# Optimization experiments

Measured on AMD Instinct MI355X. Metric: run time of the kernel, lower is better.

The kernel has to match this reference:

```python
import jax, jax.numpy as jnp
import numpy as np

B, S, H, D = 2, 2048, 16, 64
BLK_Q, BLK_K = 16, 256  # layout row-block = 16 query rows, col-block = 256 key cols


def setup_inputs() -> dict:
    key = jax.random.key(0)
    qkv = jax.random.normal(key, (B, S, 3, H, D), dtype=jnp.float32)
    nq, nk = S // BLK_Q, S // BLK_K  # 128, 8
    layout = np.zeros((nq, nk), dtype=np.int32)
    rows = np.arange(nq)
    layout[rows, (rows * BLK_Q) // BLK_K] = 1  # local diagonal block
    layout[:, 0] = 1                           # global first key block
    return {"qkv": qkv, "layout": jnp.asarray(layout)}


def reference(qkv, layout):
    # qkv: [B, S, 3, H, D], layout: [S//16, S//256] {0,1}
    b, s, _, h, d = qkv.shape
    scale = 1.0 / np.sqrt(d)  # softmax_temp defaults to 1/sqrt(d_keys)
    q = qkv[:, :, 0]  # [B,S,H,D]
    k = qkv[:, :, 1]
    v = qkv[:, :, 2]
    # Expand block layout to a dense [S, S] boolean mask
    mask = jnp.repeat(jnp.repeat(layout.astype(bool), BLK_Q, axis=0), BLK_K, axis=1)[:s, :s]
    scores = jnp.einsum('bshd,bthd->bhst', q, k) * scale  # [B,H,S,S]
    neg_inf = jnp.asarray(-jnp.inf, scores.dtype)
    scores = jnp.where(mask[None, None], scores, neg_inf)
    attn = jax.nn.softmax(scores, axis=-1)  # dropout_p = 0.0 in eval
    out = jnp.einsum('bhst,bthd->bshd', attn, v)  # [B,S,H,D]
    return out
```

## Files before the change

kernel.cpp:

```cpp
#include <hip/hip_runtime.h>

typedef float f32x4 __attribute__((ext_vector_type(4)));
typedef float f32x16 __attribute__((ext_vector_type(16)));
typedef _Float16 f16x8 __attribute__((ext_vector_type(8)));
typedef __fp16 fp16x2 __attribute__((ext_vector_type(2)));
typedef int i32x2 __attribute__((ext_vector_type(2)));

static __device__ __forceinline__ unsigned pk2(float a, float b) {
    fp16x2 r = __builtin_amdgcn_cvt_pkrtz(a, b);
    return __builtin_bit_cast(unsigned, r);
}
static __device__ __forceinline__ f16x8 pk8(float4 a, float4 b) {
    uint4 u; u.x = pk2(a.x, a.y); u.y = pk2(a.z, a.w);
    u.z = pk2(b.x, b.y); u.w = pk2(b.z, b.w);
    return __builtin_bit_cast(f16x8, u);
}

#define MFMA32(A, B, C) __builtin_amdgcn_mfma_f32_32x32x16_f16((A), (B), (C), 0, 0, 0)

__global__ __launch_bounds__(256, 2) void fba_fwd(const float* __restrict__ qkv,
                                                  const int* __restrict__ layout,
                                                  float* __restrict__ out) {
    __shared__ unsigned short Klds[2][128 * 64];
    __shared__ unsigned short Vtlds[2][64 * 128];

    const int bid = blockIdx.x;
    const int vid = (bid & 7) * 64 + (bid >> 3);
    const int b = vid >> 8;
    const int hh = (vid >> 4) & 15;
    const int j = (vid >> 1) & 7;
    const int qh = vid & 1;

    const int tid = threadIdx.x;
    const int w = tid >> 6;
    const int lane = tid & 63;
    const int l31 = lane & 31;
    const int h = lane >> 5;

    const size_t bbase = (size_t)b * 2048 * 3072;
    const int qbase = 256 * j + 128 * qh + 32 * w;

    unsigned kbl = 0; int nact = 0;
    for (int kb = 0; kb < 8; ++kb) {
        int a = 0;
        #pragma unroll
        for (int r = 0; r < 8; ++r) a |= layout[(16 * j + 8 * qh + r) * 8 + kb];
        if (a) { kbl |= (unsigned)kb << (4 * nact); ++nact; }
    }
    kbl = __builtin_amdgcn_readfirstlane(kbl);
    const int ntile = 2 * nact;

    const float SC = 0.18033688f;
    f16x8 qf[4];
    {
        const float* qp = qkv + bbase + (size_t)(qbase + l31) * 3072 + hh * 64;
        #pragma unroll
        for (int ds = 0; ds < 4; ++ds) {
            const float* p0 = qp + ds * 16 + 8 * h;
            float4 x = *(const float4*)p0;
            float4 y = *(const float4*)(p0 + 4);
            float4 xs = {x.x * SC, x.y * SC, x.z * SC, x.w * SC};
            float4 ys = {y.x * SC, y.y * SC, y.z * SC, y.w * SC};
            qf[ds] = pk8(xs, ys);
        }
    }

    f32x16 acc[2];
    acc[0] = (f32x16)(0.f);
    acc[1] = (f32x16)(0.f);
    float lsum = 0.f;

    const int skey = tid >> 4;
    const int sdc  = tid & 15;

    float4 kr0, kr1, kr2, kr3;
    float4 va0, vb0, va1, vb1;

#define STAGE_LOAD(ks_) {            \
    const float* kp_ = qkv + bbase + (size_t)((ks_) + skey) * 3072 + 1024 + hh * 64 + sdc * 4; \
    kr0 = *(const float4*)kp_;                                                      \
    kr1 = *(const float4*)(kp_ + 16 * 3072);                                        \
    kr2 = *(const float4*)(kp_ + 32 * 3072);                                        \
    kr3 = *(const float4*)(kp_ + 48 * 3072);                                        \
    const float* vp_ = qkv + bbase + (size_t)((ks_) + 2 * skey) * 3072 + 2048 + hh * 64 + sdc * 4; \
    va0 = *(const float4*)vp_;               vb0 = *(const float4*)(vp_ +      3072); \
    va1 = *(const float4*)(vp_ + 32 * 3072); vb1 = *(const float4*)(vp_ + 33 * 3072); \
}

#define WK1(m, krm, KB, koff) { int row_ = (koff) + skey + 16 * (m);                \
    *(uint2*)((char*)(KB) + ((row_ * 128 + sdc * 8) ^ ((skey & 7) << 4))) =         \
        make_uint2(pk2(krm.x, krm.y), pk2(krm.z, krm.w)); }
#define WV1(p, vam, vbm, VB, koff) {                                                \
    const float* A_ = &vam.x; const float* B_ = &vbm.x;                             \
    _Pragma("unroll")                                                               \
    for (int e2 = 0; e2 < 4; ++e2) {                                                \
        int d_ = 4 * sdc + e2;                                                      \
        int off_ = (d_ * 256 + ((koff) + 2 * skey + 32 * (p)) * 2) ^ (((d_ ^ (d_ >> 3)) & 7) << 4); \
        *(unsigned*)((char*)(VB) + off_) = pk2(A_[e2], B_[e2]);                     \
    }                                                                               \
}
#define STAGE_WRITE(nb, koff) {                                                     \
    unsigned short* KB = &Klds[nb][0];                                              \
    WK1(0, kr0, KB, koff) WK1(1, kr1, KB, koff) WK1(2, kr2, KB, koff) WK1(3, kr3, KB, koff) \
    unsigned short* VB = &Vtlds[nb][0];                                             \
    WV1(0, va0, vb0, VB, koff) WV1(1, va1, vb1, VB, koff)                           \
}

#define CHUNK(KB, VB, kt) {                                                         \
    const int key = (kt) * 32 + l31;                                                \
    const int kswz = (l31 & 7) << 4;                                                \
    f16x8 kf[4];                                                                    \
    _Pragma("unroll")                                                               \
    for (int ds = 0; ds < 4; ++ds)                                                  \
        kf[ds] = *(const f16x8*)((const char*)(KB) + ((key * 128 + ds * 32 + h * 16) ^ kswz)); \
    f16x8 vf[2][2];                                                                 \
    _Pragma("unroll")                                                               \
    for (int dt = 0; dt < 2; ++dt) {                                                \
        const int d = dt * 32 + l31;                                                \
        const int vswz = ((d ^ (d >> 3)) & 7) << 4;                                 \
        _Pragma("unroll")                                                           \
        for (int ksi = 0; ksi < 2; ++ksi)                                           \
            vf[dt][ksi] = *(const f16x8*)((const char*)(VB) + ((d * 256 + (kt) * 64 + ksi * 32 + h * 16) ^ vswz)); \
    }                                                                               \
    __builtin_amdgcn_s_setprio(1);                                                  \
    f32x16 st = (f32x16)(0.f);                                                      \
    st = MFMA32(kf[0], qf[0], st);                                                  \
    st = MFMA32(kf[1], qf[1], st);                                                  \
    st = MFMA32(kf[2], qf[2], st);                                                  \
    st = MFMA32(kf[3], qf[3], st);                                                  \
    __builtin_amdgcn_s_setprio(0);                                                  \
    unsigned ulo[4], uhi[4];                                                        \
    float psum = 0.f;                                                               \
    _Pragma("unroll")                                                               \
    for (int jq = 0; jq < 4; ++jq) {                                                \
        float e0 = exp2f(st[4 * jq + 0]), e1 = exp2f(st[4 * jq + 1]);               \
        float e2 = exp2f(st[4 * jq + 2]), e3 = exp2f(st[4 * jq + 3]);               \
        psum += (e0 + e1) + (e2 + e3);                                              \
        ulo[jq] = pk2(e0, e1); uhi[jq] = pk2(e2, e3);                               \
    }                                                                               \
    lsum += psum;                                                                   \
    __builtin_amdgcn_s_setprio(1);                                                  \
    _Pragma("unroll")                                                               \
    for (int ksi = 0; ksi < 2; ++ksi) {                                             \
        i32x2 r0 = __builtin_amdgcn_permlane32_swap((int)ulo[2 * ksi], (int)ulo[2 * ksi + 1], false, false); \
        i32x2 r1 = __builtin_amdgcn_permlane32_swap((int)uhi[2 * ksi], (int)uhi[2 * ksi + 1], false, false); \
        uint4 uw;                                                                   \
        uw.x = (unsigned)r0[0]; uw.y = (unsigned)r1[0];                             \
        uw.z = (unsigned)r0[1]; uw.w = (unsigned)r1[1];                             \
        f16x8 pf = __builtin_bit_cast(f16x8, uw);                                   \
        acc[0] = MFMA32(vf[0][ksi], pf, acc[0]);                                    \
        acc[1] = MFMA32(vf[1][ksi], pf, acc[1]);                                    \
    }                                                                               \
    __builtin_amdgcn_s_setprio(0);                                                  \
}

#define TB(t_) ((int)(((kbl >> (((t_) >> 1) * 4)) & 15) * 256 + ((t_) & 1) * 128))

    STAGE_LOAD(TB(0));
    STAGE_WRITE(0, 0);
    STAGE_LOAD(TB(0) + 64);
    STAGE_WRITE(0, 64);
    __syncthreads();

    for (int t = 0; t < ntile; ++t) {
        const bool more = (t + 1 < ntile);
        const int cur = t & 1, nxt = (t + 1) & 1;
        const unsigned short* KB = &Klds[cur][0];
        const unsigned short* VB = &Vtlds[cur][0];
        if (more) STAGE_LOAD(TB(t + 1));
        CHUNK(KB, VB, ((0 + w) & 3));
        CHUNK(KB, VB, ((1 + w) & 3));
        if (more) {
            STAGE_WRITE(nxt, 0);
            STAGE_LOAD(TB(t + 1) + 64);
        }
        CHUNK(KB, VB, ((2 + w) & 3));
        CHUNK(KB, VB, ((3 + w) & 3));
        if (more) STAGE_WRITE(nxt, 64);
        __syncthreads();
    }

    lsum += __shfl_xor(lsum, 32);
    const float inv = 1.0f / lsum;
    float* op = out + (((size_t)b * 2048 + (qbase + l31)) * 16 + hh) * 64;
    #pragma unroll
    for (int dt = 0; dt < 2; ++dt)
        #pragma unroll
        for (int jq = 0; jq < 4; ++jq) {
            float4 o;
            o.x = acc[dt][4 * jq + 0] * inv;
            o.y = acc[dt][4 * jq + 1] * inv;
            o.z = acc[dt][4 * jq + 2] * inv;
            o.w = acc[dt][4 * jq + 3] * inv;
            *(float4*)(op + dt * 32 + 8 * jq + 4 * h) = o;
        }
}

extern "C" void kernel_launch(void* const* d_in, const int* in_sizes, int n_in,
                              void* d_out, int out_size, void* d_ws, size_t ws_size,
                              hipStream_t stream) {
    const float* qkv = (const float*)d_in[0];
    const int* layout = (const int*)d_in[1];
    float* out = (float*)d_out;
    fba_fwd<<<dim3(512), dim3(256), 0, stream>>>(qkv, layout, out);
}
```

Before: 27.07 us.

## Interleave two key chunks per half-tile to overlap softmax with MFMA

Splits the per-chunk body into load, QK, softmax and PV stages, then processes two 32-key chunks together. Both QK products run back to back, and each chunk's softmax is interleaved with the other chunk's V loads and PV MFMAs. The aim is to hide exp latency behind matrix work. It also swaps exp2f for the raw hardware exp2 builtin and changes the per-wave chunk order from rotation to an XOR pattern. The cost is higher register pressure from holding two chunks' fragments and scores at once, which could hurt occupancy at 2 blocks per CU.

Result: faster. 24.33 us (-10.1%).

```diff
diff --git a/kernel.cpp b/kernel.cpp
--- a/kernel.cpp
+++ b/kernel.cpp
@@ -106,40 +106,44 @@
     WV1(0, va0, vb0, VB, koff) WV1(1, va1, vb1, VB, koff)                           \
 }
 
-#define CHUNK(KB, VB, kt) {                                                         \
-    const int key = (kt) * 32 + l31;                                                \
-    const int kswz = (l31 & 7) << 4;                                                \
-    f16x8 kf[4];                                                                    \
+#define LDK(kf, kt) {                                                               \
+    const int key_ = (kt) * 32 + l31;                                               \
+    const int ksw_ = (l31 & 7) << 4;                                                \
     _Pragma("unroll")                                                               \
     for (int ds = 0; ds < 4; ++ds)                                                  \
-        kf[ds] = *(const f16x8*)((const char*)(KB) + ((key * 128 + ds * 32 + h * 16) ^ kswz)); \
-    f16x8 vf[2][2];                                                                 \
+        kf[ds] = *(const f16x8*)((const char*)(KB) + ((key_ * 128 + ds * 32 + h * 16) ^ ksw_)); \
+}
+#define LDV(vf, kt) {                                                               \
     _Pragma("unroll")                                                               \
     for (int dt = 0; dt < 2; ++dt) {                                                \
-        const int d = dt * 32 + l31;                                                \
-        const int vswz = ((d ^ (d >> 3)) & 7) << 4;                                 \
+        const int d_ = dt * 32 + l31;                                               \
+        const int vsw_ = ((d_ ^ (d_ >> 3)) & 7) << 4;                               \
         _Pragma("unroll")                                                           \
         for (int ksi = 0; ksi < 2; ++ksi)                                           \
-            vf[dt][ksi] = *(const f16x8*)((const char*)(VB) + ((d * 256 + (kt) * 64 + ksi * 32 + h * 16) ^ vswz)); \
-    }                                                                               \
-    __builtin_amdgcn_s_setprio(1);                                                  \
-    f32x16 st = (f32x16)(0.f);                                                      \
+            vf[dt][ksi] = *(const f16x8*)((const char*)(VB) + ((d_ * 256 + (kt) * 64 + ksi * 32 + h * 16) ^ vsw_)); \
+    }                                                                               \
+}
+#define QK(st, kf) {                                                                \
+    st = (f32x16)(0.f);                                                             \
     st = MFMA32(kf[0], qf[0], st);                                                  \
     st = MFMA32(kf[1], qf[1], st);                                                  \
     st = MFMA32(kf[2], qf[2], st);                                                  \
     st = MFMA32(kf[3], qf[3], st);                                                  \
-    __builtin_amdgcn_s_setprio(0);                                                  \
-    unsigned ulo[4], uhi[4];                                                        \
-    float psum = 0.f;                                                               \
+}
+#define SM(st, ulo, uhi) {                                                          \
+    float psum_ = 0.f;                                                              \
     _Pragma("unroll")                                                               \
     for (int jq = 0; jq < 4; ++jq) {                                                \
-        float e0 = exp2f(st[4 * jq + 0]), e1 = exp2f(st[4 * jq + 1]);               \
-        float e2 = exp2f(st[4 * jq + 2]), e3 = exp2f(st[4 * jq + 3]);               \
-        psum += (e0 + e1) + (e2 + e3);                                              \
+        float e0 = __builtin_amdgcn_exp2f(st[4 * jq + 0]);                          \
+        float e1 = __builtin_amdgcn_exp2f(st[4 * jq + 1]);                          \
+        float e2 = __builtin_amdgcn_exp2f(st[4 * jq + 2]);                          \
+        float e3 = __builtin_amdgcn_exp2f(st[4 * jq + 3]);                          \
+        psum_ += (e0 + e1) + (e2 + e3);                                             \
         ulo[jq] = pk2(e0, e1); uhi[jq] = pk2(e2, e3);                               \
     }                                                                               \
-    lsum += psum;                                                                   \
-    __builtin_amdgcn_s_setprio(1);                                                  \
+    lsum += psum_;                                                                  \
+}
+#define PV(ulo, uhi, vf) {                                                          \
     _Pragma("unroll")                                                               \
     for (int ksi = 0; ksi < 2; ++ksi) {                                             \
         i32x2 r0 = __builtin_amdgcn_permlane32_swap((int)ulo[2 * ksi], (int)ulo[2 * ksi + 1], false, false); \
@@ -151,6 +155,27 @@
         acc[0] = MFMA32(vf[0][ksi], pf, acc[0]);                                    \
         acc[1] = MFMA32(vf[1][ksi], pf, acc[1]);                                    \
     }                                                                               \
+}
+
+#define HALF_BODY(ca, cb) {                                                         \
+    f16x8 kf0[4], kf1[4], vf0[2][2], vf1[2][2];                                     \
+    f32x16 st0, st1;                                                                \
+    unsigned u0lo[4], u0hi[4], u1lo[4], u1hi[4];                                    \
+    LDK(kf0, ca);                                                                   \
+    LDK(kf1, cb);                                                                   \
+    __builtin_amdgcn_s_setprio(1);                                                  \
+    QK(st0, kf0);                                                                   \
+    QK(st1, kf1);                                                                   \
+    __builtin_amdgcn_s_setprio(0);                                                  \
+    LDV(vf0, ca);                                                                   \
+    SM(st0, u0lo, u0hi);                                                            \
+    LDV(vf1, cb);                                                                   \
+    __builtin_amdgcn_s_setprio(1);                                                  \
+    PV(u0lo, u0hi, vf0);                                                            \
+    __builtin_amdgcn_s_setprio(0);                                                  \
+    SM(st1, u1lo, u1hi);                                                            \
+    __builtin_amdgcn_s_setprio(1);                                                  \
+    PV(u1lo, u1hi, vf1);                                                            \
     __builtin_amdgcn_s_setprio(0);                                                  \
 }
 
@@ -162,20 +187,19 @@
     STAGE_WRITE(0, 64);
     __syncthreads();
 
+    const int ws = w & 1;
     for (int t = 0; t < ntile; ++t) {
         const bool more = (t + 1 < ntile);
         const int cur = t & 1, nxt = (t + 1) & 1;
         const unsigned short* KB = &Klds[cur][0];
         const unsigned short* VB = &Vtlds[cur][0];
         if (more) STAGE_LOAD(TB(t + 1));
-        CHUNK(KB, VB, ((0 + w) & 3));
-        CHUNK(KB, VB, ((1 + w) & 3));
+        HALF_BODY((0 ^ ws), (1 ^ ws));
         if (more) {
             STAGE_WRITE(nxt, 0);
             STAGE_LOAD(TB(t + 1) + 64);
         }
-        CHUNK(KB, VB, ((2 + w) & 3));
-        CHUNK(KB, VB, ((3 + w) & 3));
+        HALF_BODY((2 ^ ws), (3 ^ ws));
         if (more) STAGE_WRITE(nxt, 64);
         __syncthreads();
     }
```
